# Optimization experiments

Hardware: AMD Instinct MI355X
Metric: run time of the kernel (lower is better)

Reference implementation:

```python
import jax, jax.numpy as jnp
import numpy as np

# Config: dim=768, num_heads=12, n=3 (PHM hypercomplex order)
DIM, H, NPH = 768, 12, 3
B, N = 4, 1024


def _phm_linear(x, A, S, b):
    """Parameterized-hypercomplex linear: W = sum_i kron(A[i], S[i]).
    A: (n, n, n), S: (n, out//n, in//n), b: (out,).
    kron(A_i,S_i)[a*p+c, b*q+d] = A_i[a,b] * S_i[c,d]."""
    n, p, q = S.shape
    W = jnp.einsum('iab,icd->acbd', A, S).reshape(n * p, n * q)  # (out, in)
    return x @ W.T + b


def setup_inputs() -> dict:
    key = jax.random.key(0)
    ks = jax.random.split(key, 9)
    d = DIM
    return {
        'x': jax.random.normal(ks[0], (B, N, d), dtype=jnp.float32),
        'A_qkv': jax.random.normal(ks[1], (NPH, NPH, NPH), dtype=jnp.float32) * 0.3,
        'S_qkv': jax.random.normal(ks[2], (NPH, 3 * d // NPH, d // NPH), dtype=jnp.float32) * 0.02,
        'b_qkv': jnp.zeros((3 * d,), dtype=jnp.float32),
        'A_proj': jax.random.normal(ks[3], (NPH, NPH, NPH), dtype=jnp.float32) * 0.3,
        'S_proj': jax.random.normal(ks[4], (NPH, d // NPH, d // NPH), dtype=jnp.float32) * 0.02,
        'b_proj': jnp.zeros((d,), dtype=jnp.float32),
        'W_sup': jax.random.normal(ks[5], (H, H), dtype=jnp.float32) * 0.3,
        'E_ent': jax.random.normal(ks[6], (H, H), dtype=jnp.float32) * 0.3,
    }


def reference(x, A_qkv, S_qkv, b_qkv, A_proj, S_proj, b_proj, W_sup, E_ent):
    Bn, Nn, C = x.shape
    Dh = C // H
    scale = Dh ** -0.5
    qkv = _phm_linear(x, A_qkv, S_qkv, b_qkv)                      # (B,N,3C)
    qkv = qkv.reshape(Bn, Nn, 3, H, Dh).transpose(2, 0, 3, 1, 4)   # (3,B,H,N,Dh)
    q, k, v = qkv[0], qkv[1], qkv[2]
    attn = jnp.einsum('bhnd,bhmd->bhnm', q, k) * scale             # (B,H,N,N)
    # superposition: sup[:,i] = sum_j W_sup[i,j] * attn[:,j]
    sup = jnp.einsum('ij,bjnm->binm', W_sup, attn)
    # entanglement: ent[:,i] = tanh(sup[:,i] + sum_j E[i,j]*sup[:,j])
    ent = jnp.tanh(sup + jnp.einsum('ij,bjnm->binm', E_ent, sup))
    p = jax.nn.softmax(ent, axis=-1)
    out = jnp.einsum('bhnm,bhmd->bhnd', p, v)                      # (B,H,N,Dh)
    out = out.transpose(0, 2, 1, 3).reshape(Bn, Nn, C)
    return _phm_linear(out, A_proj, S_proj, b_proj)
```

## Files before the change

### kernel.cpp

```cpp
#include <hip/hip_runtime.h>
#include <hip/hip_bf16.h>
#include <stdint.h>

typedef __attribute__((ext_vector_type(4))) float f32x4;
typedef __attribute__((ext_vector_type(8))) short bf16x8;
typedef __attribute__((ext_vector_type(2))) _Float16 f16x2;
typedef __attribute__((ext_vector_type(2))) __fp16 fp16x2;
typedef unsigned short u16;

__device__ __forceinline__ u16 f2bf(float f) {
  union { float f; uint32_t u; } v; v.f = f;
  uint32_t r = (v.u + 0x7FFFu + ((v.u >> 16) & 1u)) >> 16;
  return (u16)r;
}
__device__ __forceinline__ float bf2f(u16 u) {
  union { uint32_t i; float f; } v; v.i = ((uint32_t)u) << 16; return v.f;
}
__device__ __forceinline__ float bitsf(uint32_t u) {
  union { uint32_t i; float f; } v; v.i = u; return v.f;
}

__global__ __launch_bounds__(256) void prep_kernel(
    const float* __restrict__ x, const float* __restrict__ Aq, const float* __restrict__ Sq,
    const float* __restrict__ Ap, const float* __restrict__ Sp,
    const float* __restrict__ Wsup, const float* __restrict__ Eent,
    u16* __restrict__ xb, u16* __restrict__ wqkv, u16* __restrict__ wproj,
    float* __restrict__ m2, uint32_t* __restrict__ m2h)
{
  uint32_t id = blockIdx.x * 256u + threadIdx.x;
  if (id < 786432u) {
    float4 v = ((const float4*)x)[id];
    u16 o[4] = {f2bf(v.x), f2bf(v.y), f2bf(v.z), f2bf(v.w)};
    ((uint2*)xb)[id] = *(uint2*)o;
    return;
  }
  id -= 786432u;
  if (id < 1769472u) {
    uint32_t r = id / 768u, col = id % 768u;
    uint32_t a = r / 768u, c = r % 768u, bb = col >> 8, d = col & 255u;
    float acc = 0.f;
    #pragma unroll
    for (int i = 0; i < 3; ++i)
      acc += Aq[i*9 + a*3 + bb] * Sq[(size_t)i*196608u + c*256u + d];
    wqkv[id] = f2bf(acc);
    return;
  }
  id -= 1769472u;
  if (id < 589824u) {
    uint32_t r = id / 768u, col = id % 768u;
    uint32_t a = r >> 8, c = r & 255u, bb = col >> 8, d = col & 255u;
    float acc = 0.f;
    #pragma unroll
    for (int i = 0; i < 3; ++i)
      acc += Ap[i*9 + a*3 + bb] * Sp[(size_t)i*65536u + c*256u + d];
    wproj[id] = f2bf(acc);
    return;
  }
  id -= 589824u;
  if (id < 144u) {
    uint32_t h = id / 12u, j = id % 12u;
    float m = Wsup[h*12 + j];
    for (int tt = 0; tt < 12; ++tt) m += Eent[h*12 + tt] * Wsup[tt*12 + j];
    m2[id] = m * 0.36067376022224085f;
    return;
  }
  id -= 144u;
  if (id < 72u) {
    uint32_t h = id / 6u, j2 = id % 6u;
    float v0 = Wsup[h*12 + 2*j2], v1 = Wsup[h*12 + 2*j2 + 1];
    for (int tt = 0; tt < 12; ++tt) {
      v0 += Eent[h*12 + tt] * Wsup[tt*12 + 2*j2];
      v1 += Eent[h*12 + tt] * Wsup[tt*12 + 2*j2 + 1];
    }
    fp16x2 pk = __builtin_amdgcn_cvt_pkrtz(v0 * 0.36067376022224085f,
                                           v1 * 0.36067376022224085f);
    m2h[id] = __builtin_bit_cast(uint32_t, pk);
  }
}

template<bool BF16OUT>
__global__ __launch_bounds__(256) void gemm_bt(
    const u16* __restrict__ A, const u16* __restrict__ Bt,
    const float* __restrict__ bias, void* __restrict__ Cp,
    int M, int N, int K)
{
  __shared__ __align__(16) u16 As[128*64];
  __shared__ __align__(16) u16 Bs[128*64];
  const int t = threadIdx.x;
  const int wave = t >> 6, lane = t & 63;
  const int l15 = lane & 15, l4 = lane >> 4;
  const int bm = blockIdx.x * 128, bn = blockIdx.y * 128;
  const int wm = (wave >> 1) * 64, wn = (wave & 1) * 64;
  f32x4 acc[4][4] = {};

  for (int k0 = 0; k0 < K; k0 += 64) {
    __syncthreads();
    #pragma unroll
    for (int ro = 0; ro < 4; ++ro) {
      int L = ro*256 + wave*64 + lane;
      int row = L >> 3, cp = L & 7;
      int cl = cp ^ (row & 7);
      const u16* sa = A + (size_t)(bm + row)*K + k0 + cl*8;
      __builtin_amdgcn_global_load_lds(
        (const __attribute__((address_space(1))) uint32_t*)sa,
        (__attribute__((address_space(3))) uint32_t*)(As + (ro*256 + wave*64)*8), 16, 0, 0);
      const u16* sb = Bt + (size_t)(bn + row)*K + k0 + cl*8;
      __builtin_amdgcn_global_load_lds(
        (const __attribute__((address_space(1))) uint32_t*)sb,
        (__attribute__((address_space(3))) uint32_t*)(Bs + (ro*256 + wave*64)*8), 16, 0, 0);
    }
    asm volatile("s_waitcnt vmcnt(0)" ::: "memory");
    __syncthreads();
    #pragma unroll
    for (int kh = 0; kh < 2; ++kh) {
      bf16x8 af[4], bfr[4];
      #pragma unroll
      for (int mi = 0; mi < 4; ++mi) {
        int row = wm + mi*16 + l15;
        int ch = (kh*4 + l4) ^ (row & 7);
        af[mi] = *(const bf16x8*)(As + row*64 + ch*8);
      }
      #pragma unroll
      for (int ni = 0; ni < 4; ++ni) {
        int row = wn + ni*16 + l15;
        int ch = (kh*4 + l4) ^ (row & 7);
        bfr[ni] = *(const bf16x8*)(Bs + row*64 + ch*8);
      }
      #pragma unroll
      for (int mi = 0; mi < 4; ++mi)
        #pragma unroll
        for (int ni = 0; ni < 4; ++ni)
          acc[mi][ni] = __builtin_amdgcn_mfma_f32_16x16x32_bf16(af[mi], bfr[ni], acc[mi][ni], 0, 0, 0);
    }
  }
  #pragma unroll
  for (int mi = 0; mi < 4; ++mi) {
    #pragma unroll
    for (int ni = 0; ni < 4; ++ni) {
      int col = bn + wn + ni*16 + l15;
      float bv = bias[col];
      #pragma unroll
      for (int r = 0; r < 4; ++r) {
        int rowg = bm + wm + mi*16 + l4*4 + r;
        float v = acc[mi][ni][r] + bv;
        if (BF16OUT) ((u16*)Cp)[(size_t)rowg*N + col] = f2bf(v);
        else ((float*)Cp)[(size_t)rowg*N + col] = v;
      }
    }
  }
}

__global__ __launch_bounds__(256) void vtrans_kernel(const u16* __restrict__ qkv, u16* __restrict__ vT2)
{
  __shared__ __align__(16) u16 Lt[64][72];
  int t = threadIdx.x;
  int n0 = blockIdx.x * 64, d0 = blockIdx.y * 64, b = blockIdx.z;
  #pragma unroll
  for (int rr = 0; rr < 2; ++rr) {
    int L = rr*256 + t;
    int i = L >> 3, ch = L & 7;
    const u16* src = qkv + (size_t)(b*1024 + n0 + i)*2304 + 1536 + d0 + ch*8;
    *(uint4*)&Lt[i][ch*8] = *(const uint4*)src;
  }
  __syncthreads();
  #pragma unroll
  for (int rr = 0; rr < 2; ++rr) {
    int L = rr*256 + t;
    int oct = L >> 6, dd = L & 63;
    u16 u[8];
    #pragma unroll
    for (int r = 0; r < 8; ++r) u[r] = Lt[oct*8 + r][dd];
    *(uint4*)(vT2 + (size_t)(b*128 + (n0 >> 3) + oct)*6144 + (size_t)(d0 + dd)*8) = *(uint4*)u;
  }
}

template<int MS>
__global__ __launch_bounds__(256, 2) void attn_kernel(
    const u16* __restrict__ qkv, const u16* __restrict__ vT2,
    const uint32_t* __restrict__ M2h, u16* __restrict__ outp, float* __restrict__ Lpart)
{
  __shared__ __align__(16) u16 Qs[16*768];
  __shared__ __align__(16) u16 Ps[2*12*16*32];

  const int t = threadIdx.x;
  const int wave = t >> 6, lane = t & 63;
  const int l15 = lane & 15, l4 = lane >> 4;

  const int G = MS * 4;
  const int fid = blockIdx.x;
  const int g = fid % G, qt = fid / G;
  const int b = g & 3, ms = g >> 2;
  const int q0 = qt * 16;
  const int mbeg = ms * (1024 / MS);

  #pragma unroll
  for (int i = 0; i < 6; ++i) {
    int T = i*256 + t;
    int r = T / 96, c = T % 96;
    int cs = c ^ (r & 7);
    const u16* src = qkv + (size_t)(b*1024 + q0 + r)*2304 + cs*8;
    __builtin_amdgcn_global_load_lds(
      (const __attribute__((address_space(1))) uint32_t*)src,
      (__attribute__((address_space(3))) uint32_t*)(Qs + T*8), 16, 0, 0);
  }
  asm volatile("s_waitcnt vmcnt(0)" ::: "memory");
  __syncthreads();

  const float C1 = -2.8853900817779268f;
  const float C2 =  1.4426950408889634f;
  f32x4 oacc[3][4] = {};
  float ps_sum[3] = {0.f, 0.f, 0.f};

  for (int sit = 0; sit < (1024/MS)/64; ++sit) {
    const int mb0 = mbeg + sit*64;
    const int mb = mb0 + wave*16;

    uint32_t sp[6][4];
    const u16* krow = qkv + (size_t)(b*1024 + mb + l15)*2304 + 768 + l4*8;
    #pragma unroll
    for (int h2 = 0; h2 < 6; ++h2) {
      f32x4 s0, s1;
      {
        int h = 2*h2;
        bf16x8 qa = *(const bf16x8*)(Qs + l15*768 + ((h*8 + l4) ^ (l15 & 7))*8);
        bf16x8 qb = *(const bf16x8*)(Qs + l15*768 + ((h*8 + 4 + l4) ^ (l15 & 7))*8);
        f32x4 z = {};
        z = __builtin_amdgcn_mfma_f32_16x16x32_bf16(qa, *(const bf16x8*)(krow + h*64), z, 0, 0, 0);
        s0 = __builtin_amdgcn_mfma_f32_16x16x32_bf16(qb, *(const bf16x8*)(krow + h*64 + 32), z, 0, 0, 0);
      }
      {
        int h = 2*h2 + 1;
        bf16x8 qa = *(const bf16x8*)(Qs + l15*768 + ((h*8 + l4) ^ (l15 & 7))*8);
        bf16x8 qb = *(const bf16x8*)(Qs + l15*768 + ((h*8 + 4 + l4) ^ (l15 & 7))*8);
        f32x4 z = {};
        z = __builtin_amdgcn_mfma_f32_16x16x32_bf16(qa, *(const bf16x8*)(krow + h*64), z, 0, 0, 0);
        s1 = __builtin_amdgcn_mfma_f32_16x16x32_bf16(qb, *(const bf16x8*)(krow + h*64 + 32), z, 0, 0, 0);
      }
      #pragma unroll
      for (int r = 0; r < 4; ++r) {
        fp16x2 pk = __builtin_amdgcn_cvt_pkrtz(s0[r], s1[r]);
        sp[h2][r] = __builtin_bit_cast(uint32_t, pk);
      }
    }

    #pragma unroll
    for (int h = 0; h < 12; ++h) {
      const uint32_t* mrow = M2h + h*6;
      #pragma unroll
      for (int r = 0; r < 4; ++r) {
        float e = 0.f;
        #pragma unroll
        for (int j2 = 0; j2 < 6; ++j2)
          e = __builtin_amdgcn_fdot2(__builtin_bit_cast(f16x2, sp[j2][r]),
                                     __builtin_bit_cast(f16x2, mrow[j2]),
                                     e, false);
        float ex = __builtin_amdgcn_exp2f(e);
        float tv = __builtin_amdgcn_rcpf(ex + 1.f);
        float p  = __builtin_amdgcn_exp2f(fmaf(C1, tv, C2));
        int q = l4*4 + r;
        int c = ((wave & 1)*2 + (l15 >> 3)) ^ (q & 3);
        Ps[(((wave >> 1)*12 + h)*16 + q)*32 + c*8 + (l15 & 7)] = f2bf(p);
      }
    }
    __syncthreads();

    #pragma unroll
    for (int hh = 0; hh < 3; ++hh) {
      int h = wave*3 + hh;
      #pragma unroll
      for (int ch = 0; ch < 2; ++ch) {
        bf16x8 pf = *(const bf16x8*)(Ps + ((ch*12 + h)*16 + l15)*32 + ((l4 ^ (l15 & 3))*8));
        {
          union { bf16x8 v; uint32_t u[4]; } pc; pc.v = pf;
          float s = 0.f;
          #pragma unroll
          for (int k = 0; k < 4; ++k)
            s += bitsf(pc.u[k] & 0xFFFF0000u) + bitsf(pc.u[k] << 16);
          ps_sum[hh] += s;
        }
        const u16* vb = vT2 + (size_t)(b*128 + (mb0 >> 3) + ch*4 + l4)*6144 + (size_t)(h*64)*8;
        #pragma unroll
        for (int ci = 0; ci < 4; ++ci) {
          bf16x8 vf = *(const bf16x8*)(vb + (ci*16 + l15)*8);
          oacc[hh][ci] = __builtin_amdgcn_mfma_f32_16x16x32_bf16(pf, vf, oacc[hh][ci], 0, 0, 0);
        }
      }
    }
    __syncthreads();
  }

  #pragma unroll
  for (int hh = 0; hh < 3; ++hh) {
    ps_sum[hh] += __shfl_xor(ps_sum[hh], 16);
    ps_sum[hh] += __shfl_xor(ps_sum[hh], 32);
  }

  if (MS == 1) {
    float* Lsf = (float*)Ps;
    if (l4 == 0)
      #pragma unroll
      for (int hh = 0; hh < 3; ++hh) Lsf[(wave*3 + hh)*16 + l15] = ps_sum[hh];
    __syncthreads();
    #pragma unroll
    for (int hh = 0; hh < 3; ++hh) {
      int h = wave*3 + hh;
      #pragma unroll
      for (int r = 0; r < 4; ++r) {
        int q = l4*4 + r;
        float linv = __builtin_amdgcn_rcpf(Lsf[h*16 + q]);
        #pragma unroll
        for (int ci = 0; ci < 4; ++ci)
          outp[(size_t)(b*1024 + q0 + q)*768 + h*64 + ci*16 + l15] = f2bf(oacc[hh][ci][r] * linv);
      }
    }
  } else {
    #pragma unroll
    for (int hh = 0; hh < 3; ++hh) {
      int h = wave*3 + hh;
      #pragma unroll
      for (int r = 0; r < 4; ++r) {
        int q = l4*4 + r;
        #pragma unroll
        for (int ci = 0; ci < 4; ++ci)
          outp[((size_t)(ms*4 + b)*1024 + q0 + q)*768 + h*64 + ci*16 + l15] = f2bf(oacc[hh][ci][r]);
      }
      if (l4 == 0)
        Lpart[((ms*4 + b)*12 + h)*1024 + q0 + l15] = ps_sum[hh];
    }
  }
}

template<int MS>
__global__ __launch_bounds__(256) void merge_kernel(
    const u16* __restrict__ Opart, const float* __restrict__ Lpart, u16* __restrict__ aout)
{
  const uint32_t idx = blockIdx.x * 256u + threadIdx.x;
  const uint32_t flat = idx * 8u;
  const uint32_t b = flat / 786432u, r0 = flat % 786432u;
  const uint32_t n = r0 / 768u, c = r0 % 768u, h = c >> 6;
  float acc[8] = {};
  float l = 0.f;
  #pragma unroll
  for (int msi = 0; msi < MS; ++msi) {
    uint4 v = *(const uint4*)(Opart + ((size_t)((msi*4u + b)*1024u + n))*768u + c);
    const u16* pv = (const u16*)&v;
    #pragma unroll
    for (int k = 0; k < 8; ++k) acc[k] += bf2f(pv[k]);
    l += Lpart[((msi*4u + b)*12u + h)*1024u + n];
  }
  float linv = __builtin_amdgcn_rcpf(l);
  u16 o[8];
  #pragma unroll
  for (int k = 0; k < 8; ++k) o[k] = f2bf(acc[k] * linv);
  *(uint4*)(aout + flat) = *(uint4*)o;
}

extern "C" void kernel_launch(void* const* d_in, const int* in_sizes, int n_in,
                              void* d_out, int out_size, void* d_ws, size_t ws_size,
                              hipStream_t stream)
{
  const float* x    = (const float*)d_in[0];
  const float* Aq   = (const float*)d_in[1];
  const float* Sq   = (const float*)d_in[2];
  const float* bq   = (const float*)d_in[3];
  const float* Ap   = (const float*)d_in[4];
  const float* Sp   = (const float*)d_in[5];
  const float* bp   = (const float*)d_in[6];
  const float* Wsup = (const float*)d_in[7];
  const float* Eent = (const float*)d_in[8];

  char* ws = (char*)d_ws;
  u16*  xb    = (u16*)(ws);
  u16*  wqkv  = (u16*)(ws + 6291456);
  u16*  wproj = (u16*)(ws + 9830400);
  u16*  qkvb  = (u16*)(ws + 11010048);
  u16*  vT2   = (u16*)(ws + 29884416);
  u16*  aout  = (u16*)(ws + 36175872);
  float* m2   = (float*)(ws + 42467328);
  uint32_t* m2h = (uint32_t*)(ws + 42467904);
  const size_t base = 42468224;

  const int MS = (ws_size >= base + 4*6488064u) ? 4
               : (ws_size >= base + 2*6488064u) ? 2 : 1;
  float* Lpart = (float*)(ws + base);
  u16*   Opart = (u16*)(ws + base + (size_t)MS*196608u);

  prep_kernel<<<12289, 256, 0, stream>>>(x, Aq, Sq, Ap, Sp, Wsup, Eent, xb, wqkv, wproj, m2, m2h);
  gemm_bt<true><<<dim3(32, 18), 256, 0, stream>>>(xb, wqkv, bq, qkvb, 4096, 2304, 768);
  vtrans_kernel<<<dim3(16, 12, 4), 256, 0, stream>>>(qkvb, vT2);
  if (MS == 4) {
    attn_kernel<4><<<1024, 256, 0, stream>>>(qkvb, vT2, m2h, Opart, Lpart);
    merge_kernel<4><<<1536, 256, 0, stream>>>(Opart, Lpart, aout);
  } else if (MS == 2) {
    attn_kernel<2><<<512, 256, 0, stream>>>(qkvb, vT2, m2h, Opart, Lpart);
    merge_kernel<2><<<1536, 256, 0, stream>>>(Opart, Lpart, aout);
  } else {
    attn_kernel<1><<<256, 256, 0, stream>>>(qkvb, vT2, m2h, aout, nullptr);
  }
  gemm_bt<false><<<dim3(32, 6), 256, 0, stream>>>(aout, wproj, bp, (float*)d_out, 4096, 768, 768);
}
```

Before: 154.5 us.

## Fuse V transpose into QKV GEMM epilogue and vectorize weight prep

Removes the separate vtrans kernel: the QKV GEMM epilogue writes V columns straight into the transposed vT2 layout, which saves one launch and a read/write pass over V. The prep kernel also builds the PHM weights four columns per thread with float4 loads, so it needs fewer threads and blocks. The cost is that the fused epilogue writes V as scattered 2-byte stores at stride 8 elements, which may coalesce poorly.

```diff
diff --git a/kernel.cpp b/kernel.cpp
--- a/kernel.cpp
+++ b/kernel.cpp
@@ -35,28 +35,36 @@
     return;
   }
   id -= 786432u;
-  if (id < 1769472u) {
-    uint32_t r = id / 768u, col = id % 768u;
-    uint32_t a = r / 768u, c = r % 768u, bb = col >> 8, d = col & 255u;
-    float acc = 0.f;
-    #pragma unroll
-    for (int i = 0; i < 3; ++i)
-      acc += Aq[i*9 + a*3 + bb] * Sq[(size_t)i*196608u + c*256u + d];
-    wqkv[id] = f2bf(acc);
+  if (id < 442368u) {
+    uint32_t r = id / 192u, c4 = id % 192u, col = c4 * 4u;
+    uint32_t a = r / 768u, cc = r % 768u, bb = col >> 8, d = col & 255u;
+    float acc[4] = {};
+    #pragma unroll
+    for (int i = 0; i < 3; ++i) {
+      float co = Aq[i*9 + a*3 + bb];
+      float4 s = *(const float4*)(Sq + (size_t)i*196608u + cc*256u + d);
+      acc[0] += co * s.x; acc[1] += co * s.y; acc[2] += co * s.z; acc[3] += co * s.w;
+    }
+    u16 o[4] = {f2bf(acc[0]), f2bf(acc[1]), f2bf(acc[2]), f2bf(acc[3])};
+    ((uint2*)wqkv)[id] = *(uint2*)o;
     return;
   }
-  id -= 1769472u;
-  if (id < 589824u) {
-    uint32_t r = id / 768u, col = id % 768u;
-    uint32_t a = r >> 8, c = r & 255u, bb = col >> 8, d = col & 255u;
-    float acc = 0.f;
-    #pragma unroll
-    for (int i = 0; i < 3; ++i)
-      acc += Ap[i*9 + a*3 + bb] * Sp[(size_t)i*65536u + c*256u + d];
-    wproj[id] = f2bf(acc);
+  id -= 442368u;
+  if (id < 147456u) {
+    uint32_t r = id / 192u, c4 = id % 192u, col = c4 * 4u;
+    uint32_t a = r >> 8, cc = r & 255u, bb = col >> 8, d = col & 255u;
+    float acc[4] = {};
+    #pragma unroll
+    for (int i = 0; i < 3; ++i) {
+      float co = Ap[i*9 + a*3 + bb];
+      float4 s = *(const float4*)(Sp + (size_t)i*65536u + cc*256u + d);
+      acc[0] += co * s.x; acc[1] += co * s.y; acc[2] += co * s.z; acc[3] += co * s.w;
+    }
+    u16 o[4] = {f2bf(acc[0]), f2bf(acc[1]), f2bf(acc[2]), f2bf(acc[3])};
+    ((uint2*)wproj)[id] = *(uint2*)o;
     return;
   }
-  id -= 589824u;
+  id -= 147456u;
   if (id < 144u) {
     uint32_t h = id / 12u, j = id % 12u;
     float m = Wsup[h*12 + j];
@@ -78,10 +86,11 @@
   }
 }
 
-template<bool BF16OUT>
+template<bool BF16OUT, bool FUSEV>
 __global__ __launch_bounds__(256) void gemm_bt(
     const u16* __restrict__ A, const u16* __restrict__ Bt,
     const float* __restrict__ bias, void* __restrict__ Cp,
+    u16* __restrict__ vt2,
     int M, int N, int K)
 {
   __shared__ __align__(16) u16 As[128*64];
@@ -143,34 +152,16 @@
       for (int r = 0; r < 4; ++r) {
         int rowg = bm + wm + mi*16 + l4*4 + r;
         float v = acc[mi][ni][r] + bv;
-        if (BF16OUT) ((u16*)Cp)[(size_t)rowg*N + col] = f2bf(v);
-        else ((float*)Cp)[(size_t)rowg*N + col] = v;
-      }
-    }
-  }
-}
-
-__global__ __launch_bounds__(256) void vtrans_kernel(const u16* __restrict__ qkv, u16* __restrict__ vT2)
-{
-  __shared__ __align__(16) u16 Lt[64][72];
-  int t = threadIdx.x;
-  int n0 = blockIdx.x * 64, d0 = blockIdx.y * 64, b = blockIdx.z;
-  #pragma unroll
-  for (int rr = 0; rr < 2; ++rr) {
-    int L = rr*256 + t;
-    int i = L >> 3, ch = L & 7;
-    const u16* src = qkv + (size_t)(b*1024 + n0 + i)*2304 + 1536 + d0 + ch*8;
-    *(uint4*)&Lt[i][ch*8] = *(const uint4*)src;
-  }
-  __syncthreads();
-  #pragma unroll
-  for (int rr = 0; rr < 2; ++rr) {
-    int L = rr*256 + t;
-    int oct = L >> 6, dd = L & 63;
-    u16 u[8];
-    #pragma unroll
-    for (int r = 0; r < 8; ++r) u[r] = Lt[oct*8 + r][dd];
-    *(uint4*)(vT2 + (size_t)(b*128 + (n0 >> 3) + oct)*6144 + (size_t)(d0 + dd)*8) = *(uint4*)u;
+        if (FUSEV && col >= 1536) {
+          int d = col - 1536;
+          vt2[((size_t)((rowg >> 10)*128 + ((rowg & 1023) >> 3)))*6144 + d*8 + (rowg & 7)] = f2bf(v);
+        } else if (BF16OUT) {
+          ((u16*)Cp)[(size_t)rowg*N + col] = f2bf(v);
+        } else {
+          ((float*)Cp)[(size_t)rowg*N + col] = v;
+        }
+      }
+    }
   }
 }
 
@@ -385,9 +376,8 @@
   float* Lpart = (float*)(ws + base);
   u16*   Opart = (u16*)(ws + base + (size_t)MS*196608u);
 
-  prep_kernel<<<12289, 256, 0, stream>>>(x, Aq, Sq, Ap, Sp, Wsup, Eent, xb, wqkv, wproj, m2, m2h);
-  gemm_bt<true><<<dim3(32, 18), 256, 0, stream>>>(xb, wqkv, bq, qkvb, 4096, 2304, 768);
-  vtrans_kernel<<<dim3(16, 12, 4), 256, 0, stream>>>(qkvb, vT2);
+  prep_kernel<<<5377, 256, 0, stream>>>(x, Aq, Sq, Ap, Sp, Wsup, Eent, xb, wqkv, wproj, m2, m2h);
+  gemm_bt<true, true><<<dim3(32, 18), 256, 0, stream>>>(xb, wqkv, bq, qkvb, vT2, 4096, 2304, 768);
   if (MS == 4) {
     attn_kernel<4><<<1024, 256, 0, stream>>>(qkvb, vT2, m2h, Opart, Lpart);
     merge_kernel<4><<<1536, 256, 0, stream>>>(Opart, Lpart, aout);
@@ -397,5 +387,5 @@
   } else {
     attn_kernel<1><<<256, 256, 0, stream>>>(qkvb, vT2, m2h, aout, nullptr);
   }
-  gemm_bt<false><<<dim3(32, 6), 256, 0, stream>>>(aout, wproj, bp, (float*)d_out, 4096, 768, 768);
-}
+  gemm_bt<false, false><<<dim3(32, 6), 256, 0, stream>>>(aout, wproj, bp, (float*)d_out, nullptr, 4096, 768, 768);
+}
```

Result: faster. 141.5 us (median of 2 runs) (-8.5%).
